# Kernel optimization log

Measured on AMD Instinct MI355X. Metric: run time of the kernel, lower is better.

The kernel has to match this reference:

```python
import jax, jax.numpy as jnp
import numpy as np

B, N, D, K, H = 64, 4096, 256, 11, 512
ITERS = 5
EPS = 1e-8
LN_EPS = 1e-5  # torch LayerNorm default
SCALE = D ** -0.5


def _ln(x, w, b):
    m = jnp.mean(x, axis=-1, keepdims=True)
    v = jnp.mean(jnp.square(x - m), axis=-1, keepdims=True)
    return (x - m) * jax.lax.rsqrt(v + LN_EPS) * w + b


def setup_inputs() -> dict:
    key = jax.random.key(0)
    ks = jax.random.split(key, 16)
    s = lambda k, shp, fan: jax.random.normal(k, shp, jnp.float32) * (1.0 / np.sqrt(fan))
    return {
        "inputs": jax.random.normal(ks[0], (B, N, D), jnp.float32),
        "slots_init": jax.random.normal(ks[1], (B, K, D), jnp.float32),
        "ln_f_w": jnp.ones((D,), jnp.float32), "ln_f_b": jnp.zeros((D,), jnp.float32),
        "ln_s_w": jnp.ones((D,), jnp.float32), "ln_s_b": jnp.zeros((D,), jnp.float32),
        "ln_p_w": jnp.ones((D,), jnp.float32), "ln_p_b": jnp.zeros((D,), jnp.float32),
        "Wq": s(ks[2], (D, D), D),
        "Wk": s(ks[3], (D, D), D),
        "Wv": s(ks[4], (D, D), D),
        "W_ih": s(ks[5], (3 * D, D), D), "b_ih": jnp.zeros((3 * D,), jnp.float32),
        "W_hh": s(ks[6], (3 * D, D), D), "b_hh": jnp.zeros((3 * D,), jnp.float32),
        "W1": s(ks[7], (H, D), D), "b1": jnp.zeros((H,), jnp.float32),
        "W2": s(ks[8], (D, H), H), "b2": jnp.zeros((D,), jnp.float32),
    }


def reference(inputs, slots_init, ln_f_w, ln_f_b, ln_s_w, ln_s_b, ln_p_w, ln_p_b,
              Wq, Wk, Wv, W_ih, b_ih, W_hh, b_hh, W1, b1, W2, b2):
    x = _ln(inputs, ln_f_w, ln_f_b)              # (B, N, D)
    k = x @ Wk.T                                  # (B, N, D)
    v = x @ Wv.T                                  # (B, N, D)
    slots = slots_init                            # (B, K, D)
    for _ in range(ITERS):
        slots_prev = slots
        q = _ln(slots, ln_s_w, ln_s_b) @ Wq.T     # (B, K, D)
        dots = jnp.einsum('bid,bjd->bij', q, k) * SCALE  # (B, K, N)
        attn = jax.nn.softmax(dots, axis=1) + EPS        # softmax over slots
        attn = attn / jnp.sum(attn, axis=-1, keepdims=True)
        updates = jnp.einsum('bjd,bij->bid', v, attn)    # (B, K, D)
        # GRUCell (torch semantics)
        gi = updates @ W_ih.T + b_ih              # (B, K, 3D)
        gh = slots_prev @ W_hh.T + b_hh
        i_r, i_z, i_n = jnp.split(gi, 3, axis=-1)
        h_r, h_z, h_n = jnp.split(gh, 3, axis=-1)
        r = jax.nn.sigmoid(i_r + h_r)
        z = jax.nn.sigmoid(i_z + h_z)
        n_ = jnp.tanh(i_n + r * h_n)
        slots = (1.0 - z) * n_ + z * slots_prev
        # residual MLP
        p = _ln(slots, ln_p_w, ln_p_b)
        slots = slots + jnp.maximum(p @ W1.T + b1, 0.0) @ W2.T + b2
    return slots
```

## Files before the change

### kernel.cpp

```cpp
#include <hip/hip_runtime.h>

typedef __bf16 bf16_t;
typedef bf16_t bf16x8 __attribute__((ext_vector_type(8)));
typedef bf16_t bf16x4 __attribute__((ext_vector_type(4)));
typedef float f32x4 __attribute__((ext_vector_type(4)));

#define DEVI static __device__ __forceinline__

constexpr int BB = 64;
constexpr int NN = 4096;
constexpr int DD = 256;
constexpr int KS = 11;
constexpr int KP = 16;
constexpr int HH = 512;
constexpr float EPS_A = 1e-8f;
constexpr float LNEPS = 1e-5f;
constexpr float SCALE = 0.0625f;
constexpr int MR = BB * KP;
constexpr int NSPLIT = 8;
constexpr int ASTR = 40;

DEVI float wredf(float v) {
#pragma unroll
  for (int o = 32; o > 0; o >>= 1) v += __shfl_xor(v, o, 64);
  return v;
}

DEVI float sigm(float x) { return 1.f / (1.f + __expf(-x)); }

__global__ void prep_weights_k(
    const float* __restrict__ s0, const float* __restrict__ s1, const float* __restrict__ s2,
    const float* __restrict__ s3, const float* __restrict__ s4, const float* __restrict__ s5,
    const float* __restrict__ s6,
    bf16_t* d0, bf16_t* d1, bf16_t* d2, bf16_t* d3, bf16_t* d4, bf16_t* d5, bf16_t* d6) {
  int i = blockIdx.x * 256 + threadIdx.x;
  const float* s; bf16_t* d; int o;
  if      (i < 65536)  { s = s0; d = d0; o = i; }
  else if (i < 131072) { s = s1; d = d1; o = i - 65536; }
  else if (i < 196608) { s = s2; d = d2; o = i - 131072; }
  else if (i < 393216) { s = s3; d = d3; o = i - 196608; }
  else if (i < 589824) { s = s4; d = d4; o = i - 393216; }
  else if (i < 720896) { s = s5; d = d5; o = i - 589824; }
  else                 { s = s6; d = d6; o = i - 720896; }
  d[o] = (bf16_t)s[o];
}

__global__ void init_slots_k(const float* __restrict__ si, float* __restrict__ slots) {
  int i = blockIdx.x * 256 + threadIdx.x;
  int d = i & 255, row = i >> 8, b = row >> 4, k = row & 15;
  slots[i] = (k < KS) ? si[((long)b * KS + k) * DD + d] : 0.f;
}

__global__ void ln_inputs_k(const float* __restrict__ x, const float* __restrict__ w,
                            const float* __restrict__ bsk, bf16_t* __restrict__ o) {
  const int wvi = threadIdx.x >> 6, lane = threadIdx.x & 63;
  const long row = (long)blockIdx.x * 4 + wvi;
  const float4 v = ((const float4*)(x + row * DD))[lane];
  float s = v.x + v.y + v.z + v.w;
  float s2 = v.x * v.x + v.y * v.y + v.z * v.z + v.w * v.w;
  s = wredf(s); s2 = wredf(s2);
  const float mean = s * (1.f / DD);
  const float var = s2 * (1.f / DD) - mean * mean;
  const float rstd = rsqrtf(var + LNEPS);
  const float4 w4 = ((const float4*)w)[lane];
  const float4 b4 = ((const float4*)bsk)[lane];
  bf16x4 ov;
  ov[0] = (bf16_t)((v.x - mean) * rstd * w4.x + b4.x);
  ov[1] = (bf16_t)((v.y - mean) * rstd * w4.y + b4.y);
  ov[2] = (bf16_t)((v.z - mean) * rstd * w4.z + b4.z);
  ov[3] = (bf16_t)((v.w - mean) * rstd * w4.w + b4.w);
  ((bf16x4*)(o + row * DD))[lane] = ov;
}

template <int MODE>
__global__ __launch_bounds__(256) void gemm_big_k(const bf16_t* __restrict__ X,
                                                  const bf16_t* __restrict__ W,
                                                  bf16_t* __restrict__ out) {
  __shared__ bf16_t As[128 * 72];
  __shared__ bf16_t Bs[256 * 72];
  const bf16_t* Ap; const bf16_t* Bp;
  if (MODE == 0) { Ap = W + (long)blockIdx.y * 128 * DD; Bp = X + (long)blockIdx.x * 256 * DD; }
  else           { Ap = X + (long)blockIdx.x * 128 * DD; Bp = W; }
  const int tid = threadIdx.x;
  const int wvi = tid >> 6, lane = tid & 63;
  const int c = lane & 15, q = lane >> 4;
  const int mh = wvi >> 1, nh = wvi & 1;
  f32x4 acc[4][8];
#pragma unroll
  for (int a = 0; a < 4; a++)
#pragma unroll
    for (int b = 0; b < 8; b++) acc[a][b] = (f32x4){0.f, 0.f, 0.f, 0.f};
  for (int kb = 0; kb < DD; kb += 64) {
#pragma unroll
    for (int it = 0; it < 4; ++it) {
      int id = it * 256 + tid, r = id >> 3, ch = id & 7;
      *(bf16x8*)(As + r * 72 + ch * 8) = *(const bf16x8*)(Ap + (long)r * DD + kb + ch * 8);
    }
#pragma unroll
    for (int it = 0; it < 8; ++it) {
      int id = it * 256 + tid, r = id >> 3, ch = id & 7;
      *(bf16x8*)(Bs + r * 72 + ch * 8) = *(const bf16x8*)(Bp + (long)r * DD + kb + ch * 8);
    }
    __syncthreads();
#pragma unroll
    for (int ks = 0; ks < 2; ++ks) {
      bf16x8 af[4], bfr[8];
#pragma unroll
      for (int mt = 0; mt < 4; mt++)
        af[mt] = *(const bf16x8*)(As + (mh * 64 + mt * 16 + c) * 72 + ks * 32 + q * 8);
#pragma unroll
      for (int nt = 0; nt < 8; nt++)
        bfr[nt] = *(const bf16x8*)(Bs + (nh * 128 + nt * 16 + c) * 72 + ks * 32 + q * 8);
#pragma unroll
      for (int mt = 0; mt < 4; mt++)
#pragma unroll
        for (int nt = 0; nt < 8; nt++)
          acc[mt][nt] = __builtin_amdgcn_mfma_f32_16x16x32_bf16(af[mt], bfr[nt], acc[mt][nt], 0, 0, 0);
    }
    __syncthreads();
  }
#pragma unroll
  for (int mt = 0; mt < 4; mt++) {
#pragma unroll
    for (int nt = 0; nt < 8; nt++) {
      bf16x4 o;
#pragma unroll
      for (int r = 0; r < 4; r++) o[r] = (bf16_t)acc[mt][nt][r];
      if (MODE == 0) {
        int dg = blockIdx.y * 128 + mh * 64 + mt * 16 + q * 4;
        long ng = (long)blockIdx.x * 256 + nh * 128 + nt * 16 + c;
        *(bf16x4*)(out + ng * DD + dg) = o;
      } else {
        long ng = (long)blockIdx.x * 128 + mh * 64 + mt * 16 + q * 4;
        int d = nh * 128 + nt * 16 + c;
        long b = ng >> 12; int nin = (int)(ng & 4095);
        *(bf16x4*)(out + (b * DD + d) * NN + nin) = o;
      }
    }
  }
}

__global__ void ln_slots_k(const float* __restrict__ slots, const float* __restrict__ lw,
                           const float* __restrict__ lb, bf16_t* __restrict__ sln,
                           bf16_t* __restrict__ spl, float* __restrict__ rowsum) {
  const int row = blockIdx.x, d = threadIdx.x;
  if (row < 4) rowsum[row * 256 + d] = 0.f;
  const int kk = row & 15;
  const int idx = row * DD + d;
  if (kk >= KS) { sln[idx] = (bf16_t)0.f; spl[idx] = (bf16_t)0.f; return; }
  float v = slots[idx];
  spl[idx] = (bf16_t)v;
  __shared__ float r1[4], r2[4];
  float s = wredf(v), s2 = wredf(v * v);
  const int wvi = threadIdx.x >> 6, lane = threadIdx.x & 63;
  if (lane == 0) { r1[wvi] = s; r2[wvi] = s2; }
  __syncthreads();
  float mean = (r1[0] + r1[1] + r1[2] + r1[3]) * (1.f / DD);
  float var = (r2[0] + r2[1] + r2[2] + r2[3]) * (1.f / DD) - mean * mean;
  float rstd = rsqrtf(var + LNEPS);
  sln[idx] = (bf16_t)((v - mean) * rstd * lw[d] + lb[d]);
}

template <bool BIASF, bool RELUF, bool RESF, int OUTM>
__global__ void small_gemm_k(const bf16_t* __restrict__ A, const bf16_t* __restrict__ W,
                             const float* __restrict__ bias, const float* __restrict__ res,
                             void* __restrict__ out, int C, int Kd) {
  const int lane = threadIdx.x & 63, c = lane & 15, q = lane >> 4;
  const int wid = blockIdx.x * 4 + (threadIdx.x >> 6);
  const int nct = C >> 4;
  const int mt = wid / nct, ct = wid % nct;
  const bf16_t* ap = A + (long)(mt * 16 + c) * Kd + q * 8;
  const bf16_t* wp = W + (long)(ct * 16 + c) * Kd + q * 8;
  f32x4 acc = (f32x4){0.f, 0.f, 0.f, 0.f};
  for (int k0 = 0; k0 < Kd; k0 += 32)
    acc = __builtin_amdgcn_mfma_f32_16x16x32_bf16(*(const bf16x8*)(ap + k0),
                                                  *(const bf16x8*)(wp + k0), acc, 0, 0, 0);
  const int col = ct * 16 + c;
  const float bv = BIASF ? bias[col] : 0.f;
#pragma unroll
  for (int r = 0; r < 4; r++) {
    const int row = mt * 16 + q * 4 + r;
    float v = acc[r] + bv;
    if (RELUF) v = fmaxf(v, 0.f);
    if (RESF) v += res[(long)row * C + col];
    if (OUTM == 0) ((float*)out)[(long)row * C + col] = v;
    else if (OUTM == 1) ((bf16_t*)out)[(long)row * C + col] = (bf16_t)v;
    else {
      int b = row >> 4, k2 = row & 15;
      if (k2 < KS) ((float*)out)[((long)b * KS + k2) * C + col] = v;
    }
  }
}

__global__ __launch_bounds__(256) void fused_attn_k(const bf16_t* __restrict__ q_bf,
                                                    const bf16_t* __restrict__ k_bf,
                                                    const bf16_t* __restrict__ vT_bf,
                                                    float* __restrict__ upd_part,
                                                    float* __restrict__ rowsum) {
  const int b = blockIdx.x >> 3, sp = blockIdx.x & 7;
  const int wvi = threadIdx.x >> 6, lane = threadIdx.x & 63;
  const int c = lane & 15, q = lane >> 4;

  __shared__ bf16_t att_s[4][16 * ASTR];
  bf16_t* as = att_s[wvi];

  const bf16_t* qp = q_bf + (long)b * KP * DD;
  bf16x8 af[8];
#pragma unroll
  for (int kc = 0; kc < 8; kc++) af[kc] = *(const bf16x8*)(qp + c * DD + kc * 32 + q * 8);

  f32x4 pacc[16];
#pragma unroll
  for (int dt = 0; dt < 16; dt++) pacc[dt] = (f32x4){0.f, 0.f, 0.f, 0.f};
  float rs[4] = {0.f, 0.f, 0.f, 0.f};

  const int n_base = sp * (NN / NSPLIT) + wvi * 128;
  const bf16_t* kp = k_bf + (long)b * NN * DD;
  const bf16_t* vp = vT_bf + (long)b * DD * NN;

  for (int ch = 0; ch < 4; ++ch) {
    const int n0 = n_base + ch * 32;
    float v[2][4];
#pragma unroll
    for (int t = 0; t < 2; t++) {
      f32x4 dacc = (f32x4){0.f, 0.f, 0.f, 0.f};
      const bf16_t* bp = kp + (long)(n0 + t * 16 + c) * DD + q * 8;
#pragma unroll
      for (int kc = 0; kc < 8; kc++)
        dacc = __builtin_amdgcn_mfma_f32_16x16x32_bf16(af[kc], *(const bf16x8*)(bp + kc * 32),
                                                       dacc, 0, 0, 0);
#pragma unroll
      for (int r = 0; r < 4; r++) {
        float dv = dacc[r] * SCALE;
        if (q * 4 + r >= KS) dv = -1e30f;
        v[t][r] = dv;
      }
      float m4 = fmaxf(fmaxf(v[t][0], v[t][1]), fmaxf(v[t][2], v[t][3]));
      m4 = fmaxf(m4, __shfl_xor(m4, 16, 64));
      m4 = fmaxf(m4, __shfl_xor(m4, 32, 64));
      float s4 = 0.f;
#pragma unroll
      for (int r = 0; r < 4; r++) { v[t][r] = __expf(v[t][r] - m4); s4 += v[t][r]; }
      s4 += __shfl_xor(s4, 16, 64);
      s4 += __shfl_xor(s4, 32, 64);
      const float inv = 1.f / s4;
#pragma unroll
      for (int r = 0; r < 4; r++) {
        float a = v[t][r] * inv + EPS_A;
        rs[r] += a;
        as[(q * 4 + r) * ASTR + t * 16 + c] = (bf16_t)a;
      }
    }
    bf16x8 pa = *(const bf16x8*)(as + c * ASTR + q * 8);
#pragma unroll
    for (int dt = 0; dt < 16; dt++) {
      const bf16_t* bp2 = vp + (long)(dt * 16 + c) * NN + n0 + q * 8;
      pacc[dt] = __builtin_amdgcn_mfma_f32_16x16x32_bf16(pa, *(const bf16x8*)(bp2),
                                                         pacc[dt], 0, 0, 0);
    }
  }

#pragma unroll
  for (int off = 1; off < 16; off <<= 1)
#pragma unroll
    for (int r = 0; r < 4; r++) rs[r] += __shfl_xor(rs[r], off, 64);
  if (c == 0) {
#pragma unroll
    for (int r = 0; r < 4; r++) atomicAdd(&rowsum[b * KP + q * 4 + r], rs[r]);
  }

  float* up = upd_part + ((long)blockIdx.x * 4 + wvi) * (KP * DD);
#pragma unroll
  for (int dt = 0; dt < 16; dt++)
#pragma unroll
    for (int r = 0; r < 4; r++) up[(q * 4 + r) * DD + dt * 16 + c] = pacc[dt][r];
}

__global__ void finalize_k(const float* __restrict__ upd_part, const float* __restrict__ rowsum,
                           bf16_t* __restrict__ o) {
  const int i = blockIdx.x * 256 + threadIdx.x;
  const int row = i >> 8, d = i & 255, b = row >> 4, kk = row & 15;
  const float* up = upd_part + (long)b * 32 * (KP * DD) + kk * DD + d;
  float s = 0.f;
#pragma unroll
  for (int w = 0; w < 32; w++) s += up[(long)w * (KP * DD)];
  float v = (kk < KS) ? s / rowsum[row] : 0.f;
  o[i] = (bf16_t)v;
}

__global__ void gru_ln_k(const float* __restrict__ gi, const float* __restrict__ gh,
                         const float* __restrict__ sin_, const float* __restrict__ lw,
                         const float* __restrict__ lb, float* __restrict__ sout,
                         bf16_t* __restrict__ pbf) {
  const int row = blockIdx.x, d = threadIdx.x;
  const int kk = row & 15;
  const int idx = row * DD + d;
  if (kk >= KS) { sout[idx] = 0.f; pbf[idx] = (bf16_t)0.f; return; }
  const long g = (long)row * 768;
  float r = sigm(gi[g + d] + gh[g + d]);
  float z = sigm(gi[g + 256 + d] + gh[g + 256 + d]);
  float nn = tanhf(gi[g + 512 + d] + r * gh[g + 512 + d]);
  float sp = sin_[idx];
  float s = (1.f - z) * nn + z * sp;
  sout[idx] = s;
  __shared__ float r1[4], r2[4];
  float su = wredf(s), sq = wredf(s * s);
  const int wvi = threadIdx.x >> 6, lane = threadIdx.x & 63;
  if (lane == 0) { r1[wvi] = su; r2[wvi] = sq; }
  __syncthreads();
  float mean = (r1[0] + r1[1] + r1[2] + r1[3]) * (1.f / DD);
  float var = (r2[0] + r2[1] + r2[2] + r2[3]) * (1.f / DD) - mean * mean;
  float rstd = rsqrtf(var + LNEPS);
  pbf[idx] = (bf16_t)((s - mean) * rstd * lw[d] + lb[d]);
}

extern "C" void kernel_launch(void* const* d_in, const int* in_sizes, int n_in, void* d_out,
                              int out_size, void* d_ws, size_t ws_size, hipStream_t stream) {
  (void)in_sizes; (void)n_in; (void)out_size; (void)ws_size;
  const float* inputs = (const float*)d_in[0];
  const float* slots_in = (const float*)d_in[1];
  const float* ln_f_w = (const float*)d_in[2];
  const float* ln_f_b = (const float*)d_in[3];
  const float* ln_s_w = (const float*)d_in[4];
  const float* ln_s_b = (const float*)d_in[5];
  const float* ln_p_w = (const float*)d_in[6];
  const float* ln_p_b = (const float*)d_in[7];
  const float* Wq = (const float*)d_in[8];
  const float* Wk = (const float*)d_in[9];
  const float* Wv = (const float*)d_in[10];
  const float* W_ih = (const float*)d_in[11];
  const float* b_ih = (const float*)d_in[12];
  const float* W_hh = (const float*)d_in[13];
  const float* b_hh = (const float*)d_in[14];
  const float* W1 = (const float*)d_in[15];
  const float* b1 = (const float*)d_in[16];
  const float* W2 = (const float*)d_in[17];
  const float* b2 = (const float*)d_in[18];

  char* p = (char*)d_ws;
  auto alloc = [&](size_t bytes) { char* r = p; p += (bytes + 255) & ~(size_t)255; return r; };
  bf16_t* x_bf  = (bf16_t*)alloc((size_t)BB * NN * DD * 2);
  bf16_t* k_bf  = (bf16_t*)alloc((size_t)BB * NN * DD * 2);
  bf16_t* vT_bf = (bf16_t*)alloc((size_t)BB * NN * DD * 2);
  bf16_t* Wq_bf = (bf16_t*)alloc(65536 * 2);
  bf16_t* Wk_bf = (bf16_t*)alloc(65536 * 2);
  bf16_t* Wv_bf = (bf16_t*)alloc(65536 * 2);
  bf16_t* Wih_bf = (bf16_t*)alloc(196608 * 2);
  bf16_t* Whh_bf = (bf16_t*)alloc(196608 * 2);
  bf16_t* W1_bf = (bf16_t*)alloc(131072 * 2);
  bf16_t* W2_bf = (bf16_t*)alloc(131072 * 2);
  float* slots = (float*)alloc((size_t)MR * DD * 4);
  bf16_t* sln = (bf16_t*)alloc((size_t)MR * DD * 2);
  bf16_t* spl = (bf16_t*)alloc((size_t)MR * DD * 2);
  bf16_t* q_bf = (bf16_t*)alloc((size_t)MR * DD * 2);
  float* upd_part = (float*)alloc((size_t)BB * 32 * KP * DD * 4);
  float* rowsum = (float*)alloc((size_t)MR * 4);
  bf16_t* upd_bf = (bf16_t*)alloc((size_t)MR * DD * 2);
  float* gi = (float*)alloc((size_t)MR * 768 * 4);
  float* gh = (float*)alloc((size_t)MR * 768 * 4);
  bf16_t* pbf = (bf16_t*)alloc((size_t)MR * DD * 2);
  bf16_t* h1 = (bf16_t*)alloc((size_t)MR * HH * 2);

  prep_weights_k<<<3328, 256, 0, stream>>>(Wq, Wk, Wv, W_ih, W_hh, W1, W2, Wq_bf, Wk_bf, Wv_bf,
                                           Wih_bf, Whh_bf, W1_bf, W2_bf);
  init_slots_k<<<1024, 256, 0, stream>>>(slots_in, slots);
  ln_inputs_k<<<65536, 256, 0, stream>>>(inputs, ln_f_w, ln_f_b, x_bf);
  gemm_big_k<0><<<dim3(1024, 2), 256, 0, stream>>>(x_bf, Wk_bf, k_bf);
  gemm_big_k<1><<<dim3(2048, 1), 256, 0, stream>>>(x_bf, Wv_bf, vT_bf);

  for (int t = 0; t < 5; t++) {
    ln_slots_k<<<1024, 256, 0, stream>>>(slots, ln_s_w, ln_s_b, sln, spl, rowsum);
    small_gemm_k<false, false, false, 1><<<256, 256, 0, stream>>>(sln, Wq_bf, nullptr, nullptr, q_bf, 256, 256);
    fused_attn_k<<<BB * NSPLIT, 256, 0, stream>>>(q_bf, k_bf, vT_bf, upd_part, rowsum);
    finalize_k<<<1024, 256, 0, stream>>>(upd_part, rowsum, upd_bf);
    small_gemm_k<true, false, false, 0><<<768, 256, 0, stream>>>(upd_bf, Wih_bf, b_ih, nullptr, gi, 768, 256);
    small_gemm_k<true, false, false, 0><<<768, 256, 0, stream>>>(spl, Whh_bf, b_hh, nullptr, gh, 768, 256);
    gru_ln_k<<<1024, 256, 0, stream>>>(gi, gh, slots, ln_p_w, ln_p_b, slots, pbf);
    small_gemm_k<true, true, false, 1><<<512, 256, 0, stream>>>(pbf, W1_bf, b1, nullptr, h1, 512, 256);
    if (t < 4)
      small_gemm_k<true, false, true, 0><<<256, 256, 0, stream>>>(h1, W2_bf, b2, slots, slots, 256, 512);
    else
      small_gemm_k<true, false, true, 2><<<256, 256, 0, stream>>>(h1, W2_bf, b2, slots, d_out, 256, 512);
  }
}
```

Before: 1.209 ms.

## Fuse per-iteration slot update into one per-batch kernel and merge K/V GEMMs

Replaces the chain of small kernels run each iteration (slot LN, q projection, finalize, two GRU GEMMs, GRU+LN, two MLP GEMMs) with a single per-batch kernel that keeps the slots in shared memory and runs the whole GRU, MLP and next q projection with MFMA. The attention kernel now sums its four wave partials in shared memory, so the partial buffer shrinks from 32 to 8 slices per batch. The K and V projection GEMMs are merged into one launch. This cuts launch count and global round trips, but the fused kernel runs only 64 blocks, so each block loads all of its weights from global memory with low occupancy.

Measured after the change: 1.346 ms. +11.3%, slower.

```diff
diff --git a/kernel.cpp b/kernel.cpp
--- a/kernel.cpp
+++ b/kernel.cpp
@@ -6,13 +6,13 @@
 typedef float f32x4 __attribute__((ext_vector_type(4)));
 
 #define DEVI static __device__ __forceinline__
+#define MFMA16(a, b, c) __builtin_amdgcn_mfma_f32_16x16x32_bf16((a), (b), (c), 0, 0, 0)
 
 constexpr int BB = 64;
 constexpr int NN = 4096;
 constexpr int DD = 256;
 constexpr int KS = 11;
 constexpr int KP = 16;
-constexpr int HH = 512;
 constexpr float EPS_A = 1e-8f;
 constexpr float LNEPS = 1e-5f;
 constexpr float SCALE = 0.0625f;
@@ -43,12 +43,6 @@
   else if (i < 720896) { s = s5; d = d5; o = i - 589824; }
   else                 { s = s6; d = d6; o = i - 720896; }
   d[o] = (bf16_t)s[o];
-}
-
-__global__ void init_slots_k(const float* __restrict__ si, float* __restrict__ slots) {
-  int i = blockIdx.x * 256 + threadIdx.x;
-  int d = i & 255, row = i >> 8, b = row >> 4, k = row & 15;
-  slots[i] = (k < KS) ? si[((long)b * KS + k) * DD + d] : 0.f;
 }
 
 __global__ void ln_inputs_k(const float* __restrict__ x, const float* __restrict__ w,
@@ -72,15 +66,20 @@
   ((bf16x4*)(o + row * DD))[lane] = ov;
 }
 
-template <int MODE>
-__global__ __launch_bounds__(256) void gemm_big_k(const bf16_t* __restrict__ X,
-                                                  const bf16_t* __restrict__ W,
-                                                  bf16_t* __restrict__ out) {
+__global__ __launch_bounds__(256) void gemm_kv_k(const bf16_t* __restrict__ X,
+                                                 const bf16_t* __restrict__ Wk,
+                                                 const bf16_t* __restrict__ Wv,
+                                                 bf16_t* __restrict__ kout,
+                                                 bf16_t* __restrict__ vout) {
   __shared__ bf16_t As[128 * 72];
   __shared__ bf16_t Bs[256 * 72];
+  const int bid = blockIdx.x;
+  int mode, bx, by;
+  if (bid < 2048) { mode = 0; bx = bid & 1023; by = bid >> 10; }
+  else            { mode = 1; bx = bid - 2048; by = 0; }
   const bf16_t* Ap; const bf16_t* Bp;
-  if (MODE == 0) { Ap = W + (long)blockIdx.y * 128 * DD; Bp = X + (long)blockIdx.x * 256 * DD; }
-  else           { Ap = X + (long)blockIdx.x * 128 * DD; Bp = W; }
+  if (mode == 0) { Ap = Wk + (long)by * 128 * DD; Bp = X + (long)bx * 256 * DD; }
+  else           { Ap = X + (long)bx * 128 * DD; Bp = Wv; }
   const int tid = threadIdx.x;
   const int wvi = tid >> 6, lane = tid & 63;
   const int c = lane & 15, q = lane >> 4;
@@ -115,7 +114,7 @@
       for (int mt = 0; mt < 4; mt++)
 #pragma unroll
         for (int nt = 0; nt < 8; nt++)
-          acc[mt][nt] = __builtin_amdgcn_mfma_f32_16x16x32_bf16(af[mt], bfr[nt], acc[mt][nt], 0, 0, 0);
+          acc[mt][nt] = MFMA16(af[mt], bfr[nt], acc[mt][nt]);
     }
     __syncthreads();
   }
@@ -126,68 +125,16 @@
       bf16x4 o;
 #pragma unroll
       for (int r = 0; r < 4; r++) o[r] = (bf16_t)acc[mt][nt][r];
-      if (MODE == 0) {
-        int dg = blockIdx.y * 128 + mh * 64 + mt * 16 + q * 4;
-        long ng = (long)blockIdx.x * 256 + nh * 128 + nt * 16 + c;
-        *(bf16x4*)(out + ng * DD + dg) = o;
+      if (mode == 0) {
+        int dg = by * 128 + mh * 64 + mt * 16 + q * 4;
+        long ng = (long)bx * 256 + nh * 128 + nt * 16 + c;
+        *(bf16x4*)(kout + ng * DD + dg) = o;
       } else {
-        long ng = (long)blockIdx.x * 128 + mh * 64 + mt * 16 + q * 4;
+        long ng = (long)bx * 128 + mh * 64 + mt * 16 + q * 4;
         int d = nh * 128 + nt * 16 + c;
         long b = ng >> 12; int nin = (int)(ng & 4095);
-        *(bf16x4*)(out + (b * DD + d) * NN + nin) = o;
-      }
-    }
-  }
-}
-
-__global__ void ln_slots_k(const float* __restrict__ slots, const float* __restrict__ lw,
-                           const float* __restrict__ lb, bf16_t* __restrict__ sln,
-                           bf16_t* __restrict__ spl, float* __restrict__ rowsum) {
-  const int row = blockIdx.x, d = threadIdx.x;
-  if (row < 4) rowsum[row * 256 + d] = 0.f;
-  const int kk = row & 15;
-  const int idx = row * DD + d;
-  if (kk >= KS) { sln[idx] = (bf16_t)0.f; spl[idx] = (bf16_t)0.f; return; }
-  float v = slots[idx];
-  spl[idx] = (bf16_t)v;
-  __shared__ float r1[4], r2[4];
-  float s = wredf(v), s2 = wredf(v * v);
-  const int wvi = threadIdx.x >> 6, lane = threadIdx.x & 63;
-  if (lane == 0) { r1[wvi] = s; r2[wvi] = s2; }
-  __syncthreads();
-  float mean = (r1[0] + r1[1] + r1[2] + r1[3]) * (1.f / DD);
-  float var = (r2[0] + r2[1] + r2[2] + r2[3]) * (1.f / DD) - mean * mean;
-  float rstd = rsqrtf(var + LNEPS);
-  sln[idx] = (bf16_t)((v - mean) * rstd * lw[d] + lb[d]);
-}
-
-template <bool BIASF, bool RELUF, bool RESF, int OUTM>
-__global__ void small_gemm_k(const bf16_t* __restrict__ A, const bf16_t* __restrict__ W,
-                             const float* __restrict__ bias, const float* __restrict__ res,
-                             void* __restrict__ out, int C, int Kd) {
-  const int lane = threadIdx.x & 63, c = lane & 15, q = lane >> 4;
-  const int wid = blockIdx.x * 4 + (threadIdx.x >> 6);
-  const int nct = C >> 4;
-  const int mt = wid / nct, ct = wid % nct;
-  const bf16_t* ap = A + (long)(mt * 16 + c) * Kd + q * 8;
-  const bf16_t* wp = W + (long)(ct * 16 + c) * Kd + q * 8;
-  f32x4 acc = (f32x4){0.f, 0.f, 0.f, 0.f};
-  for (int k0 = 0; k0 < Kd; k0 += 32)
-    acc = __builtin_amdgcn_mfma_f32_16x16x32_bf16(*(const bf16x8*)(ap + k0),
-                                                  *(const bf16x8*)(wp + k0), acc, 0, 0, 0);
-  const int col = ct * 16 + c;
-  const float bv = BIASF ? bias[col] : 0.f;
-#pragma unroll
-  for (int r = 0; r < 4; r++) {
-    const int row = mt * 16 + q * 4 + r;
-    float v = acc[r] + bv;
-    if (RELUF) v = fmaxf(v, 0.f);
-    if (RESF) v += res[(long)row * C + col];
-    if (OUTM == 0) ((float*)out)[(long)row * C + col] = v;
-    else if (OUTM == 1) ((bf16_t*)out)[(long)row * C + col] = (bf16_t)v;
-    else {
-      int b = row >> 4, k2 = row & 15;
-      if (k2 < KS) ((float*)out)[((long)b * KS + k2) * C + col] = v;
+        *(bf16x4*)(vout + (b * DD + d) * NN + nin) = o;
+      }
     }
   }
 }
@@ -202,6 +149,7 @@
   const int c = lane & 15, q = lane >> 4;
 
   __shared__ bf16_t att_s[4][16 * ASTR];
+  __shared__ float sP[4][KP * DD];
   bf16_t* as = att_s[wvi];
 
   const bf16_t* qp = q_bf + (long)b * KP * DD;
@@ -227,8 +175,7 @@
       const bf16_t* bp = kp + (long)(n0 + t * 16 + c) * DD + q * 8;
 #pragma unroll
       for (int kc = 0; kc < 8; kc++)
-        dacc = __builtin_amdgcn_mfma_f32_16x16x32_bf16(af[kc], *(const bf16x8*)(bp + kc * 32),
-                                                       dacc, 0, 0, 0);
+        dacc = MFMA16(af[kc], *(const bf16x8*)(bp + kc * 32), dacc);
 #pragma unroll
       for (int r = 0; r < 4; r++) {
         float dv = dacc[r] * SCALE;
@@ -255,8 +202,7 @@
 #pragma unroll
     for (int dt = 0; dt < 16; dt++) {
       const bf16_t* bp2 = vp + (long)(dt * 16 + c) * NN + n0 + q * 8;
-      pacc[dt] = __builtin_amdgcn_mfma_f32_16x16x32_bf16(pa, *(const bf16x8*)(bp2),
-                                                         pacc[dt], 0, 0, 0);
+      pacc[dt] = MFMA16(pa, *(const bf16x8*)(bp2), pacc[dt]);
     }
   }
 
@@ -269,49 +215,196 @@
     for (int r = 0; r < 4; r++) atomicAdd(&rowsum[b * KP + q * 4 + r], rs[r]);
   }
 
-  float* up = upd_part + ((long)blockIdx.x * 4 + wvi) * (KP * DD);
 #pragma unroll
   for (int dt = 0; dt < 16; dt++)
 #pragma unroll
-    for (int r = 0; r < 4; r++) up[(q * 4 + r) * DD + dt * 16 + c] = pacc[dt][r];
-}
-
-__global__ void finalize_k(const float* __restrict__ upd_part, const float* __restrict__ rowsum,
-                           bf16_t* __restrict__ o) {
-  const int i = blockIdx.x * 256 + threadIdx.x;
-  const int row = i >> 8, d = i & 255, b = row >> 4, kk = row & 15;
-  const float* up = upd_part + (long)b * 32 * (KP * DD) + kk * DD + d;
-  float s = 0.f;
-#pragma unroll
-  for (int w = 0; w < 32; w++) s += up[(long)w * (KP * DD)];
-  float v = (kk < KS) ? s / rowsum[row] : 0.f;
-  o[i] = (bf16_t)v;
-}
-
-__global__ void gru_ln_k(const float* __restrict__ gi, const float* __restrict__ gh,
-                         const float* __restrict__ sin_, const float* __restrict__ lw,
-                         const float* __restrict__ lb, float* __restrict__ sout,
-                         bf16_t* __restrict__ pbf) {
-  const int row = blockIdx.x, d = threadIdx.x;
-  const int kk = row & 15;
-  const int idx = row * DD + d;
-  if (kk >= KS) { sout[idx] = 0.f; pbf[idx] = (bf16_t)0.f; return; }
-  const long g = (long)row * 768;
-  float r = sigm(gi[g + d] + gh[g + d]);
-  float z = sigm(gi[g + 256 + d] + gh[g + 256 + d]);
-  float nn = tanhf(gi[g + 512 + d] + r * gh[g + 512 + d]);
-  float sp = sin_[idx];
-  float s = (1.f - z) * nn + z * sp;
-  sout[idx] = s;
-  __shared__ float r1[4], r2[4];
-  float su = wredf(s), sq = wredf(s * s);
-  const int wvi = threadIdx.x >> 6, lane = threadIdx.x & 63;
-  if (lane == 0) { r1[wvi] = su; r2[wvi] = sq; }
+    for (int r = 0; r < 4; r++) sP[wvi][(q * 4 + r) * DD + dt * 16 + c] = pacc[dt][r];
   __syncthreads();
-  float mean = (r1[0] + r1[1] + r1[2] + r1[3]) * (1.f / DD);
-  float var = (r2[0] + r2[1] + r2[2] + r2[3]) * (1.f / DD) - mean * mean;
-  float rstd = rsqrtf(var + LNEPS);
-  pbf[idx] = (bf16_t)((s - mean) * rstd * lw[d] + lb[d]);
+  float* up = upd_part + (long)blockIdx.x * (KP * DD);
+  for (int idx = threadIdx.x; idx < KP * DD; idx += 256)
+    up[idx] = sP[0][idx] + sP[1][idx] + sP[2][idx] + sP[3][idx];
+}
+
+template <int MODE>
+__global__ __launch_bounds__(256, 1) void slot_update_k(
+    const float* __restrict__ slots_init, float* __restrict__ slots_g,
+    const float* __restrict__ upd_part, float* __restrict__ rowsum,
+    bf16_t* __restrict__ q_bf, float* __restrict__ d_out,
+    const bf16_t* __restrict__ Wq, const bf16_t* __restrict__ Wih,
+    const bf16_t* __restrict__ Whh, const bf16_t* __restrict__ W1,
+    const bf16_t* __restrict__ W2,
+    const float* __restrict__ b_ih, const float* __restrict__ b_hh,
+    const float* __restrict__ b1, const float* __restrict__ b2,
+    const float* __restrict__ ln_s_w, const float* __restrict__ ln_s_b,
+    const float* __restrict__ ln_p_w, const float* __restrict__ ln_p_b) {
+  const int b = blockIdx.x;
+  const int tid = threadIdx.x, w = tid >> 6, lane = tid & 63;
+  const int c = lane & 15, q = lane >> 4;
+
+  __shared__ float sS[16][264];
+  __shared__ bf16_t sA1[16 * 272];
+  __shared__ bf16_t sA2[16 * 528];
+  __shared__ float sMu[16], sRs[16];
+
+  float* slots_b = slots_g + (long)b * KP * DD;
+
+  auto rowstats = [&]() {
+    __syncthreads();
+    int row = w * 4 + q;
+    float sm = 0.f, sq2 = 0.f;
+#pragma unroll
+    for (int i = 0; i < 16; i++) { float v = sS[row][i * 16 + c]; sm += v; sq2 += v * v; }
+#pragma unroll
+    for (int o = 1; o < 16; o <<= 1) { sm += __shfl_xor(sm, o, 64); sq2 += __shfl_xor(sq2, o, 64); }
+    if (c == 0) {
+      float mu = sm * (1.f / 256.f);
+      float var = sq2 * (1.f / 256.f) - mu * mu;
+      sMu[row] = mu; sRs[row] = rsqrtf(var + LNEPS);
+    }
+    __syncthreads();
+  };
+
+  if constexpr (MODE == 0) {
+    for (int idx = tid; idx < KP * DD; idx += 256) {
+      int row = idx >> 8, d = idx & 255;
+      float v = (row < KS) ? slots_init[((long)b * KS + row) * DD + d] : 0.f;
+      sS[row][d] = v;
+      slots_b[idx] = v;
+    }
+  } else {
+    for (int idx = tid; idx < KP * DD; idx += 256) {
+      int row = idx >> 8, d = idx & 255;
+      float sv = slots_b[idx];
+      sS[row][d] = sv;
+      sA2[row * 272 + d] = (bf16_t)sv;
+      float s = 0.f;
+      const float* up = upd_part + ((long)b * 8) * (KP * DD) + idx;
+#pragma unroll
+      for (int p = 0; p < 8; p++) s += up[(long)p * (KP * DD)];
+      sA1[row * 272 + d] = (bf16_t)(s / rowsum[b * KP + row]);
+    }
+    __syncthreads();
+
+    f32x4 air[4], aiz[4], ain[4], ahr[4], ahz[4], ahn[4];
+#pragma unroll
+    for (int j = 0; j < 4; j++) {
+      air[j] = (f32x4){0.f, 0.f, 0.f, 0.f}; aiz[j] = air[j]; ain[j] = air[j];
+      ahr[j] = air[j]; ahz[j] = air[j]; ahn[j] = air[j];
+    }
+    for (int k0 = 0; k0 < 256; k0 += 32) {
+      bf16x8 aU = *(const bf16x8*)(sA1 + c * 272 + k0 + q * 8);
+      bf16x8 aS = *(const bf16x8*)(sA2 + c * 272 + k0 + q * 8);
+#pragma unroll
+      for (int j = 0; j < 4; j++) {
+        const long colr = (w * 4 + j) * 16 + c;
+        air[j] = MFMA16(aU, *(const bf16x8*)(Wih + colr * 256 + k0 + q * 8), air[j]);
+        aiz[j] = MFMA16(aU, *(const bf16x8*)(Wih + (colr + 256) * 256 + k0 + q * 8), aiz[j]);
+        ain[j] = MFMA16(aU, *(const bf16x8*)(Wih + (colr + 512) * 256 + k0 + q * 8), ain[j]);
+        ahr[j] = MFMA16(aS, *(const bf16x8*)(Whh + colr * 256 + k0 + q * 8), ahr[j]);
+        ahz[j] = MFMA16(aS, *(const bf16x8*)(Whh + (colr + 256) * 256 + k0 + q * 8), ahz[j]);
+        ahn[j] = MFMA16(aS, *(const bf16x8*)(Whh + (colr + 512) * 256 + k0 + q * 8), ahn[j]);
+      }
+    }
+#pragma unroll
+    for (int j = 0; j < 4; j++) {
+      const int colr = (w * 4 + j) * 16 + c;
+      const float bir = b_ih[colr], biz = b_ih[colr + 256], bin = b_ih[colr + 512];
+      const float bhr = b_hh[colr], bhz = b_hh[colr + 256], bhn = b_hh[colr + 512];
+#pragma unroll
+      for (int r = 0; r < 4; r++) {
+        const int row = q * 4 + r;
+        float rg = sigm(air[j][r] + bir + ahr[j][r] + bhr);
+        float zg = sigm(aiz[j][r] + biz + ahz[j][r] + bhz);
+        float ng = tanhf(ain[j][r] + bin + rg * (ahn[j][r] + bhn));
+        float sp = sS[row][colr];
+        sS[row][colr] = (1.f - zg) * ng + zg * sp;
+      }
+    }
+
+    rowstats();
+    for (int idx = tid; idx < KP * DD; idx += 256) {
+      int row = idx >> 8, d = idx & 255;
+      sA1[row * 272 + d] = (bf16_t)((sS[row][d] - sMu[row]) * sRs[row] * ln_p_w[d] + ln_p_b[d]);
+    }
+    __syncthreads();
+
+    f32x4 h[8];
+#pragma unroll
+    for (int j = 0; j < 8; j++) h[j] = (f32x4){0.f, 0.f, 0.f, 0.f};
+    for (int k0 = 0; k0 < 256; k0 += 32) {
+      bf16x8 aP = *(const bf16x8*)(sA1 + c * 272 + k0 + q * 8);
+#pragma unroll
+      for (int j = 0; j < 8; j++) {
+        const long col = (w * 8 + j) * 16 + c;
+        h[j] = MFMA16(aP, *(const bf16x8*)(W1 + col * 256 + k0 + q * 8), h[j]);
+      }
+    }
+#pragma unroll
+    for (int j = 0; j < 8; j++) {
+      const int col = (w * 8 + j) * 16 + c;
+      const float bb = b1[col];
+#pragma unroll
+      for (int r = 0; r < 4; r++)
+        sA2[(q * 4 + r) * 528 + col] = (bf16_t)fmaxf(h[j][r] + bb, 0.f);
+    }
+    __syncthreads();
+
+    f32x4 m4[4];
+#pragma unroll
+    for (int j = 0; j < 4; j++) m4[j] = (f32x4){0.f, 0.f, 0.f, 0.f};
+    for (int k0 = 0; k0 < 512; k0 += 32) {
+      bf16x8 aH = *(const bf16x8*)(sA2 + c * 528 + k0 + q * 8);
+#pragma unroll
+      for (int j = 0; j < 4; j++) {
+        const long col = (w * 4 + j) * 16 + c;
+        m4[j] = MFMA16(aH, *(const bf16x8*)(W2 + col * 512 + k0 + q * 8), m4[j]);
+      }
+    }
+#pragma unroll
+    for (int j = 0; j < 4; j++) {
+      const int col = (w * 4 + j) * 16 + c;
+      const float bb = b2[col];
+#pragma unroll
+      for (int r = 0; r < 4; r++) {
+        const int row = q * 4 + r;
+        float sfin = m4[j][r] + bb + sS[row][col];
+        if constexpr (MODE == 2) {
+          if (row < KS) d_out[((long)b * KS + row) * DD + col] = sfin;
+        } else {
+          sS[row][col] = sfin;
+          slots_b[row * DD + col] = sfin;
+        }
+      }
+    }
+    if constexpr (MODE == 2) return;
+  }
+
+  rowstats();
+  for (int idx = tid; idx < KP * DD; idx += 256) {
+    int row = idx >> 8, d = idx & 255;
+    sA1[row * 272 + d] = (bf16_t)((sS[row][d] - sMu[row]) * sRs[row] * ln_s_w[d] + ln_s_b[d]);
+  }
+  __syncthreads();
+
+  f32x4 qa[4];
+#pragma unroll
+  for (int j = 0; j < 4; j++) qa[j] = (f32x4){0.f, 0.f, 0.f, 0.f};
+  for (int k0 = 0; k0 < 256; k0 += 32) {
+    bf16x8 aL = *(const bf16x8*)(sA1 + c * 272 + k0 + q * 8);
+#pragma unroll
+    for (int j = 0; j < 4; j++) {
+      const long col = (w * 4 + j) * 16 + c;
+      qa[j] = MFMA16(aL, *(const bf16x8*)(Wq + col * 256 + k0 + q * 8), qa[j]);
+    }
+  }
+  bf16_t* qb = q_bf + (long)b * KP * DD;
+#pragma unroll
+  for (int j = 0; j < 4; j++) {
+    const int col = (w * 4 + j) * 16 + c;
+#pragma unroll
+    for (int r = 0; r < 4; r++) qb[(q * 4 + r) * DD + col] = (bf16_t)qa[j][r];
+  }
+  if (tid < KP) rowsum[b * KP + tid] = 0.f;
 }
 
 extern "C" void kernel_launch(void* const* d_in, const int* in_sizes, int n_in, void* d_out,
@@ -350,36 +443,28 @@
   bf16_t* W1_bf = (bf16_t*)alloc(131072 * 2);
   bf16_t* W2_bf = (bf16_t*)alloc(131072 * 2);
   float* slots = (float*)alloc((size_t)MR * DD * 4);
-  bf16_t* sln = (bf16_t*)alloc((size_t)MR * DD * 2);
-  bf16_t* spl = (bf16_t*)alloc((size_t)MR * DD * 2);
   bf16_t* q_bf = (bf16_t*)alloc((size_t)MR * DD * 2);
-  float* upd_part = (float*)alloc((size_t)BB * 32 * KP * DD * 4);
+  float* upd_part = (float*)alloc((size_t)BB * NSPLIT * KP * DD * 4);
   float* rowsum = (float*)alloc((size_t)MR * 4);
-  bf16_t* upd_bf = (bf16_t*)alloc((size_t)MR * DD * 2);
-  float* gi = (float*)alloc((size_t)MR * 768 * 4);
-  float* gh = (float*)alloc((size_t)MR * 768 * 4);
-  bf16_t* pbf = (bf16_t*)alloc((size_t)MR * DD * 2);
-  bf16_t* h1 = (bf16_t*)alloc((size_t)MR * HH * 2);
 
   prep_weights_k<<<3328, 256, 0, stream>>>(Wq, Wk, Wv, W_ih, W_hh, W1, W2, Wq_bf, Wk_bf, Wv_bf,
                                            Wih_bf, Whh_bf, W1_bf, W2_bf);
-  init_slots_k<<<1024, 256, 0, stream>>>(slots_in, slots);
+  slot_update_k<0><<<BB, 256, 0, stream>>>(slots_in, slots, upd_part, rowsum, q_bf, nullptr,
+                                           Wq_bf, Wih_bf, Whh_bf, W1_bf, W2_bf,
+                                           b_ih, b_hh, b1, b2, ln_s_w, ln_s_b, ln_p_w, ln_p_b);
   ln_inputs_k<<<65536, 256, 0, stream>>>(inputs, ln_f_w, ln_f_b, x_bf);
-  gemm_big_k<0><<<dim3(1024, 2), 256, 0, stream>>>(x_bf, Wk_bf, k_bf);
-  gemm_big_k<1><<<dim3(2048, 1), 256, 0, stream>>>(x_bf, Wv_bf, vT_bf);
+  gemm_kv_k<<<4096, 256, 0, stream>>>(x_bf, Wk_bf, Wv_bf, k_bf, vT_bf);
 
   for (int t = 0; t < 5; t++) {
-    ln_slots_k<<<1024, 256, 0, stream>>>(slots, ln_s_w, ln_s_b, sln, spl, rowsum);
-    small_gemm_k<false, false, false, 1><<<256, 256, 0, stream>>>(sln, Wq_bf, nullptr, nullptr, q_bf, 256, 256);
     fused_attn_k<<<BB * NSPLIT, 256, 0, stream>>>(q_bf, k_bf, vT_bf, upd_part, rowsum);
-    finalize_k<<<1024, 256, 0, stream>>>(upd_part, rowsum, upd_bf);
-    small_gemm_k<true, false, false, 0><<<768, 256, 0, stream>>>(upd_bf, Wih_bf, b_ih, nullptr, gi, 768, 256);
-    small_gemm_k<true, false, false, 0><<<768, 256, 0, stream>>>(spl, Whh_bf, b_hh, nullptr, gh, 768, 256);
-    gru_ln_k<<<1024, 256, 0, stream>>>(gi, gh, slots, ln_p_w, ln_p_b, slots, pbf);
-    small_gemm_k<true, true, false, 1><<<512, 256, 0, stream>>>(pbf, W1_bf, b1, nullptr, h1, 512, 256);
     if (t < 4)
-      small_gemm_k<true, false, true, 0><<<256, 256, 0, stream>>>(h1, W2_bf, b2, slots, slots, 256, 512);
+      slot_update_k<1><<<BB, 256, 0, stream>>>(slots_in, slots, upd_part, rowsum, q_bf, nullptr,
+                                               Wq_bf, Wih_bf, Whh_bf, W1_bf, W2_bf,
+                                               b_ih, b_hh, b1, b2, ln_s_w, ln_s_b, ln_p_w, ln_p_b);
     else
-      small_gemm_k<true, false, true, 2><<<256, 256, 0, stream>>>(h1, W2_bf, b2, slots, d_out, 256, 512);
-  }
-}
+      slot_update_k<2><<<BB, 256, 0, stream>>>(slots_in, slots, upd_part, rowsum, q_bf,
+                                               (float*)d_out,
+                                               Wq_bf, Wih_bf, Whh_bf, W1_bf, W2_bf,
+                                               b_ih, b_hh, b1, b2, ln_s_w, ln_s_b, ln_p_w, ln_p_b);
+  }
+}
```
